# Kernel optimization log

Measured on AMD Instinct MI355X. Metric: run time of the kernel, lower is better.

## Reference

```python
import jax, jax.numpy as jnp
import numpy as np

B, H, W, C, D = 32, 28, 28, 768, 64  # batch, height, width, input_dim, adapter dim
EMB = 64  # meta_net output / layer_embedding size


def qgelu(x):
    return x * jax.nn.sigmoid(1.702 * x)


def setup_inputs() -> dict:
    key = jax.random.key(0)
    ks = jax.random.split(key, 10)
    s = 0.02
    return {
        "x": jax.random.normal(ks[0], (B, H, W, C), jnp.float32),
        "meta_w1": jax.random.normal(ks[1], (EMB, C), jnp.float32) * s,
        "meta_b1": jnp.zeros((EMB,), jnp.float32),
        "meta_w2": jax.random.normal(ks[2], (EMB, EMB), jnp.float32) * s,
        "meta_b2": jnp.zeros((EMB,), jnp.float32),
        "layer_emb": jax.random.normal(ks[3], (EMB,), jnp.float32),
        "hyper_w": jax.random.normal(ks[4], (D * D * 9, EMB), jnp.float32) * s,
        "hyper_b": jnp.zeros((D * D * 9,), jnp.float32),
        "down_w": jax.random.normal(ks[5], (D, C), jnp.float32) * np.sqrt(6.0 / (C + D)),
        "down_b": jnp.zeros((D,), jnp.float32),
        "up_w": jax.random.normal(ks[6], (C, D), jnp.float32) * s,  # torch inits zeros; random for nontrivial test
        "up_b": jnp.zeros((C,), jnp.float32),
    }


def reference(x, meta_w1, meta_b1, meta_w2, meta_b2, layer_emb,
              hyper_w, hyper_b, down_w, down_b, up_w, up_b):
    # meta_net: Linear -> ReLU -> Linear, then mean over (H, W)
    h = jax.nn.relu(jnp.einsum('bhwc,oc->bhwo', x, meta_w1) + meta_b1)
    prompt = (jnp.einsum('bhwo,po->bhwp', h, meta_w2) + meta_b2).mean(axis=(1, 2))  # [B, EMB]
    # fuse_type == 'add'
    fused = layer_emb[None, :] + prompt  # [B, EMB]
    # hypernet -> per-sample conv weights [B, D, D, 3, 3]
    conv_w = (fused @ hyper_w.T + hyper_b).reshape(-1, D, D, 3, 3)
    # adapter_down + QuickGELU
    x_down = jnp.einsum('bhwc,dc->bhwd', x, down_w) + down_b  # [B,H,W,D]
    x_patch = qgelu(x_down).transpose(0, 3, 1, 2)  # [B,D,H,W]
    # per-sample 3x3 conv, stride 1, padding 1 (vmapped over batch)
    def conv1(xi, wi):
        return jax.lax.conv_general_dilated(xi[None], wi, (1, 1), [(1, 1), (1, 1)])[0]
    y = jax.vmap(conv1)(x_patch, conv_w)  # [B,D,H,W]
    y = qgelu(y.transpose(0, 2, 3, 1))  # [B,H,W,D]; dropout is identity in eval
    return jnp.einsum('bhwd,cd->bhwc', y, up_w) + up_b
```

## Files before the change

### kernel.cpp

```cpp
#include <hip/hip_runtime.h>
#include <math.h>

#define B_    32
#define H_    28
#define W_    28
#define C_    768
#define D_    64
#define EMB_  64
#define HW_   (H_ * W_)
#define NPOS  (B_ * HW_)
#define CWROWS (D_ * D_ * 9)

typedef __attribute__((ext_vector_type(8))) short bf16x8;
typedef __attribute__((ext_vector_type(4))) float f32x4;

__device__ __forceinline__ float qgelu(float v) {
    return v / (1.f + __expf(-1.702f * v));
}
__device__ __forceinline__ float relu(float v) { return fmaxf(v, 0.f); }

__device__ __forceinline__ ushort f2bf(float f) {
    union { float f; unsigned u; } v; v.f = f;
    return (ushort)((v.u + 0x7fffu + ((v.u >> 16) & 1u)) >> 16);
}

__device__ __forceinline__ void* swz(void* base, int row, int kbyte) {
    return (void*)((char*)base + row * 128 + (kbyte ^ ((row & 7) << 4)));
}

typedef const __attribute__((address_space(1))) void g_void;
typedef __attribute__((address_space(3))) void l_void;
__device__ __forceinline__ void gload16(const void* g, void* l) {
    __builtin_amdgcn_global_load_lds((g_void*)g, (l_void*)l, 16, 0, 0);
}

__global__ void k_cvt(const float* __restrict__ w1, const float* __restrict__ dw,
                      const float* __restrict__ uw,
                      ushort* __restrict__ wcat2, ushort* __restrict__ wup2)
{
    const int f = (blockIdx.x * 256 + threadIdx.x) * 4;
    float4 v;
    size_t dst;
    ushort* base;
    if (f < 98304) {
        int n, k;
        if (f < 49152) { n = f / 768;            k = f % 768; v = *(const float4*)(w1 + (size_t)n * 768 + k); }
        else           { int g = f - 49152; n = 64 + g / 768; k = g % 768; v = *(const float4*)(dw + (size_t)(n - 64) * 768 + k); }
        const int kb = k >> 6, kk = k & 63;
        dst  = (size_t)kb * 8192 + n * 64 + (kk ^ ((n & 7) << 3));
        base = wcat2;
    } else {
        const int g = f - 98304;
        const int n = g >> 6, kk = g & 63;
        v = *(const float4*)(uw + g);
        dst  = (size_t)n * 64 + (kk ^ ((n & 7) << 3));
        base = wup2;
    }
    union { ushort u[4]; uint2 p; } o;
    o.u[0] = f2bf(v.x); o.u[1] = f2bf(v.y); o.u[2] = f2bf(v.z); o.u[3] = f2bf(v.w);
    *(uint2*)(base + dst) = o.p;
}

__global__ __launch_bounds__(256)
void k_gemm_md(const float* __restrict__ x, const ushort* __restrict__ wcat2,
               const float* __restrict__ b1, const float* __restrict__ db,
               float* __restrict__ hbuf, ushort* __restrict__ xact)
{
    __shared__ ushort As[32 * 64];
    __shared__ ushort Bs[128 * 64];
    const int t = threadIdx.x;
    const int wid = t >> 6, lane = t & 63;
    const int lo = lane & 15, hi = lane >> 4;
    const int bm = blockIdx.x;

    f32x4 acc[2][2] = {};

    const int arow = t >> 3, akq = t & 7;
    const float* asrc = x + (size_t)(bm * 32 + arow) * C_ + akq * 8;

    float4 p0 = *(const float4*)(asrc);
    float4 p1 = *(const float4*)(asrc + 4);

    for (int k0 = 0; k0 < C_; k0 += 64) {
        __syncthreads();
        {
            union { ushort u[8]; float4 v; } tmp;
            tmp.u[0] = f2bf(p0.x); tmp.u[1] = f2bf(p0.y);
            tmp.u[2] = f2bf(p0.z); tmp.u[3] = f2bf(p0.w);
            tmp.u[4] = f2bf(p1.x); tmp.u[5] = f2bf(p1.y);
            tmp.u[6] = f2bf(p1.z); tmp.u[7] = f2bf(p1.w);
            *(float4*)swz(As, arow, akq * 16) = tmp.v;
        }
        {
            const ushort* bsrc = wcat2 + (size_t)(k0 >> 6) * 8192;
            #pragma unroll
            for (int c = 0; c < 4; ++c) {
                const int cbase = (wid * 4 + c) * 512;
                gload16(bsrc + cbase + lane * 8, (ushort*)Bs + cbase);
            }
        }
        if (k0 + 64 < C_) {
            p0 = *(const float4*)(asrc + k0 + 64);
            p1 = *(const float4*)(asrc + k0 + 68);
        }
        __syncthreads();

        #pragma unroll
        for (int ks = 0; ks < 2; ++ks) {
            bf16x8 a[2], b[2];
            #pragma unroll
            for (int i = 0; i < 2; ++i)
                a[i] = *(const bf16x8*)swz(As, i * 16 + lo, ks * 64 + hi * 16);
            #pragma unroll
            for (int j = 0; j < 2; ++j)
                b[j] = *(const bf16x8*)swz(Bs, wid * 32 + j * 16 + lo, ks * 64 + hi * 16);
            #pragma unroll
            for (int i = 0; i < 2; ++i)
                #pragma unroll
                for (int j = 0; j < 2; ++j)
                    acc[i][j] = __builtin_amdgcn_mfma_f32_16x16x32_bf16(a[i], b[j], acc[i][j], 0, 0, 0);
        }
    }

    #pragma unroll
    for (int j = 0; j < 2; ++j) {
        const int n = wid * 32 + j * 16 + lo;
        if (n < 64) {
            const float bias = b1[n];
            #pragma unroll
            for (int i = 0; i < 2; ++i)
                #pragma unroll
                for (int r = 0; r < 4; ++r) {
                    int pos = bm * 32 + i * 16 + hi * 4 + r;
                    hbuf[(size_t)pos * 64 + n] = relu(acc[i][j][r] + bias);
                }
        } else {
            const float bias = db[n - 64];
            #pragma unroll
            for (int i = 0; i < 2; ++i)
                #pragma unroll
                for (int r = 0; r < 4; ++r) {
                    int pos = bm * 32 + i * 16 + hi * 4 + r;
                    xact[(size_t)pos * 64 + (n - 64)] = f2bf(qgelu(acc[i][j][r] + bias));
                }
        }
    }
}

__global__ void k_reduce1(const float* __restrict__ hbuf, float* __restrict__ partial)
{
    __shared__ float part[16][EMB_];
    const int b = blockIdx.x, q = blockIdx.y;
    const int tid = threadIdx.x;
    const int e4 = tid & 15, pc = tid >> 4;

    const float* base = hbuf + ((size_t)b * HW_ + q * 196) * 64 + e4 * 4;
    float4 acc = make_float4(0.f, 0.f, 0.f, 0.f);
    for (int i = pc; i < 196; i += 16) {
        float4 v = *(const float4*)(base + (size_t)i * 64);
        acc.x += v.x; acc.y += v.y; acc.z += v.z; acc.w += v.w;
    }
    part[pc][e4 * 4 + 0] = acc.x;
    part[pc][e4 * 4 + 1] = acc.y;
    part[pc][e4 * 4 + 2] = acc.z;
    part[pc][e4 * 4 + 3] = acc.w;
    __syncthreads();
    if (tid < EMB_) {
        float s = 0.f;
        #pragma unroll
        for (int c = 0; c < 16; ++c) s += part[c][tid];
        partial[(size_t)(b * 4 + q) * EMB_ + tid] = s;
    }
}

__global__ void k_hyper(const float* __restrict__ partial, const float* __restrict__ layer_emb,
                        const float* __restrict__ w2, const float* __restrict__ b2,
                        const float* __restrict__ hyper_w, const float* __restrict__ hyper_b,
                        ushort* __restrict__ cwb)
{
    __shared__ float w2L[64][65];
    __shared__ float hmL[8][EMB_];
    __shared__ float fusedL[8][EMB_];
    const int tid = threadIdx.x;
    const int b0 = blockIdx.y * 8;

    for (int i = tid; i < 1024; i += 256) {
        int r = i >> 4, c = (i & 15) * 4;
        float4 v = *(const float4*)(w2 + (size_t)r * 64 + c);
        w2L[r][c] = v.x; w2L[r][c + 1] = v.y; w2L[r][c + 2] = v.z; w2L[r][c + 3] = v.w;
    }
    for (int i = tid; i < 512; i += 256) {
        int bl = i >> 6, e = i & 63;
        const float* pp = partial + (size_t)((b0 + bl) * 4) * EMB_ + e;
        float s = pp[0] + pp[64] + pp[128] + pp[192];
        hmL[bl][e] = s * (1.f / HW_);
    }
    __syncthreads();
    for (int i = tid; i < 512; i += 256) {
        int bl = i >> 6, e = i & 63;
        float a0 = 0.f, a1 = 0.f, a2 = 0.f, a3 = 0.f;
        #pragma unroll
        for (int k = 0; k < EMB_; k += 4) {
            a0 = fmaf(hmL[bl][k + 0], w2L[e][k + 0], a0);
            a1 = fmaf(hmL[bl][k + 1], w2L[e][k + 1], a1);
            a2 = fmaf(hmL[bl][k + 2], w2L[e][k + 2], a2);
            a3 = fmaf(hmL[bl][k + 3], w2L[e][k + 3], a3);
        }
        fusedL[bl][e] = (a0 + a1) + (a2 + a3) + b2[e] + layer_emb[e];
    }
    __syncthreads();

    const int f    = blockIdx.x * 256 + tid;
    const int din  = f & 63;
    const int dout = (f >> 6) & 63;
    const int tap  = f >> 12;
    const int r    = (dout * 64 + din) * 9 + tap;

    float wrow[EMB_];
    const float4* hw4 = (const float4*)(hyper_w + (size_t)r * EMB_);
    #pragma unroll
    for (int i = 0; i < EMB_ / 4; ++i) {
        float4 v = hw4[i];
        wrow[i*4+0] = v.x; wrow[i*4+1] = v.y; wrow[i*4+2] = v.z; wrow[i*4+3] = v.w;
    }
    const float hb = hyper_b[r];

    for (int bl = 0; bl < 8; ++bl) {
        float a0 = 0.f, a1 = 0.f, a2 = 0.f, a3 = 0.f;
        #pragma unroll
        for (int i = 0; i < EMB_; i += 4) {
            a0 = fmaf(fusedL[bl][i+0], wrow[i+0], a0);
            a1 = fmaf(fusedL[bl][i+1], wrow[i+1], a1);
            a2 = fmaf(fusedL[bl][i+2], wrow[i+2], a2);
            a3 = fmaf(fusedL[bl][i+3], wrow[i+3], a3);
        }
        cwb[(size_t)(b0 + bl) * CWROWS + f] = f2bf((a0 + a1) + (a2 + a3) + hb);
    }
}

__global__ __launch_bounds__(512)
void k_convup(const ushort* __restrict__ xact, const ushort* __restrict__ cwb,
              const ushort* __restrict__ wup2, const float* __restrict__ ub,
              float* __restrict__ out)
{
    __shared__ ushort wsl[192 * 64];
    __shared__ ushort xs[34 * 64];
    const int t = threadIdx.x;
    const int lane = t & 63;
    const int lo = lane & 15, hi = lane >> 4;
    const int b = blockIdx.x / H_;
    const int h = blockIdx.x % H_;
    const int mw = (t >> 6) >> 2;
    const int nw = (t >> 6) & 3;
    const int w0 = mw * 16;

    f32x4 acc = {};

    for (int kh = 0; kh < 3; ++kh) {
        const int hh = h + kh - 1;
        __syncthreads();
        const ushort* wsrc = cwb + (size_t)b * CWROWS + (size_t)kh * 3 * 4096;
        #pragma unroll
        for (int s = 0; s < 3; ++s) {
            int j = s * 512 + t;
            *(float4*)swz(wsl, j >> 3, (j & 7) * 16) = *(const float4*)(wsrc + j * 8);
        }
        if (t < 272) {
            int c = t >> 3, kseg = t & 7;
            int w = c - 1;
            float4 v = make_float4(0.f, 0.f, 0.f, 0.f);
            if (hh >= 0 && hh < H_ && w >= 0 && w < W_)
                v = *(const float4*)(xact + ((size_t)((b * H_ + hh) * W_) + w) * 64 + kseg * 8);
            *(float4*)swz(xs, c, kseg * 16) = v;
        }
        __syncthreads();
        #pragma unroll
        for (int kw = 0; kw < 3; ++kw) {
            #pragma unroll
            for (int ks = 0; ks < 2; ++ks) {
                bf16x8 a  = *(const bf16x8*)swz(xs, w0 + lo + kw, ks * 64 + hi * 16);
                bf16x8 bf = *(const bf16x8*)swz(wsl, kw * 64 + nw * 16 + lo, ks * 64 + hi * 16);
                acc = __builtin_amdgcn_mfma_f32_16x16x32_bf16(a, bf, acc, 0, 0, 0);
            }
        }
    }

    __syncthreads();
    ushort* yt = xs;
    const int dout = nw * 16 + lo;
    #pragma unroll
    for (int r = 0; r < 4; ++r) {
        int w = w0 + hi * 4 + r;
        *(ushort*)swz(yt, w, dout * 2) = f2bf(qgelu(acc[r]));
    }
    __syncthreads();

    bf16x8 af[2];
    #pragma unroll
    for (int ks = 0; ks < 2; ++ks)
        af[ks] = *(const bf16x8*)swz(yt, mw * 16 + lo, ks * 64 + hi * 16);

    ushort* Bs = wsl;
    const size_t pos0 = (size_t)(b * H_ + h) * W_;

    for (int nc = 0; nc < 6; ++nc) {
        {
            const ushort* bsrc = wup2 + (size_t)nc * 8192;
            const int wid = t >> 6;
            #pragma unroll
            for (int c = 0; c < 2; ++c) {
                const int cbase = (wid * 2 + c) * 512;
                gload16(bsrc + cbase + lane * 8, Bs + cbase);
            }
        }
        __syncthreads();

        f32x4 uacc[2] = {};
        #pragma unroll
        for (int ks = 0; ks < 2; ++ks) {
            bf16x8 bb[2];
            #pragma unroll
            for (int j = 0; j < 2; ++j)
                bb[j] = *(const bf16x8*)swz(Bs, nw * 32 + j * 16 + lo, ks * 64 + hi * 16);
            #pragma unroll
            for (int j = 0; j < 2; ++j)
                uacc[j] = __builtin_amdgcn_mfma_f32_16x16x32_bf16(af[ks], bb[j], uacc[j], 0, 0, 0);
        }

        #pragma unroll
        for (int j = 0; j < 2; ++j) {
            const int n = nc * 128 + nw * 32 + j * 16 + lo;
            const float bias = ub[n];
            #pragma unroll
            for (int r = 0; r < 4; ++r) {
                int m = mw * 16 + hi * 4 + r;
                if (m < W_)
                    out[(pos0 + m) * C_ + n] = uacc[j][r] + bias;
            }
        }
        __syncthreads();
    }
}

extern "C" void kernel_launch(void* const* d_in, const int* in_sizes, int n_in,
                              void* d_out, int out_size, void* d_ws, size_t ws_size,
                              hipStream_t stream) {
    const float* x         = (const float*)d_in[0];
    const float* meta_w1   = (const float*)d_in[1];
    const float* meta_b1   = (const float*)d_in[2];
    const float* meta_w2   = (const float*)d_in[3];
    const float* meta_b2   = (const float*)d_in[4];
    const float* layer_emb = (const float*)d_in[5];
    const float* hyper_w   = (const float*)d_in[6];
    const float* hyper_b   = (const float*)d_in[7];
    const float* down_w    = (const float*)d_in[8];
    const float* down_b    = (const float*)d_in[9];
    const float* up_w      = (const float*)d_in[10];
    const float* up_b      = (const float*)d_in[11];
    float* out = (float*)d_out;

    char* p = (char*)d_ws;
    float*  hbuf    = (float*)p;           p += (size_t)NPOS * 64 * 4;
    ushort* xact    = (ushort*)p;          p += (size_t)NPOS * 64 * 2;
    float*  partial = (float*)p;           p += (size_t)B_ * 4 * EMB_ * 4;
    ushort* cwb     = (ushort*)p;          p += (size_t)B_ * CWROWS * 2;
    ushort* wcat2   = (ushort*)p;          p += (size_t)128 * C_ * 2;
    ushort* wup2    = (ushort*)p;

    k_cvt<<<144, 256, 0, stream>>>(meta_w1, down_w, up_w, wcat2, wup2);
    k_gemm_md<<<NPOS / 32, 256, 0, stream>>>(x, wcat2, meta_b1, down_b, hbuf, xact);
    k_reduce1<<<dim3(B_, 4), 256, 0, stream>>>(hbuf, partial);
    dim3 hgrid(CWROWS / 256, B_ / 8);
    k_hyper<<<hgrid, 256, 0, stream>>>(partial, layer_emb, meta_w2, meta_b2,
                                       hyper_w, hyper_b, cwb);
    k_convup<<<B_ * H_, 512, 0, stream>>>(xact, cwb, wup2, up_b, out);
}
```

Before: 70.44 us.

## Double-buffer LDS tiles in down-projection GEMM and up-projection loop

Adds ping-pong shared-memory buffers to the first GEMM kernel and to the up-projection stage of the conv kernel. The next K tile or N chunk is prefetched into the alternate buffer while MFMAs run on the current one, which halves the barriers per iteration and hides global load latency. In exchange it uses more LDS per block, which may lower occupancy, especially in k_convup where an extra 16KB buffer is added.

Measured after the change: 74.93 us. 1.06x slower.

```diff
diff --git a/kernel.cpp b/kernel.cpp
--- a/kernel.cpp
+++ b/kernel.cpp
@@ -61,13 +61,53 @@
     *(uint2*)(base + dst) = o.p;
 }
 
+#define GEMM_STEP(KT, CA, CB, NA, NB)                                              \
+    {                                                                               \
+        __syncthreads();                                                            \
+        const bool more = (KT) < 11;                                                \
+        float4 q0, q1;                                                              \
+        if (more) {                                                                 \
+            q0 = *(const float4*)(asrc + ((KT) + 1) * 64);                          \
+            q1 = *(const float4*)(asrc + ((KT) + 1) * 64 + 4);                      \
+            const ushort* bsrc = wcat2 + (size_t)((KT) + 1) * 8192;                 \
+            _Pragma("unroll")                                                       \
+            for (int c = 0; c < 4; ++c) {                                           \
+                const int cb = (wid * 4 + c) * 512;                                 \
+                gload16(bsrc + cb + lane * 8, (ushort*)(NB) + cb);                  \
+            }                                                                       \
+        }                                                                           \
+        _Pragma("unroll")                                                           \
+        for (int ks = 0; ks < 2; ++ks) {                                            \
+            bf16x8 a[2], b[2];                                                      \
+            _Pragma("unroll")                                                       \
+            for (int i = 0; i < 2; ++i)                                             \
+                a[i] = *(const bf16x8*)swz((CA), i * 16 + lo, ks * 64 + hi * 16);   \
+            _Pragma("unroll")                                                       \
+            for (int j = 0; j < 2; ++j)                                             \
+                b[j] = *(const bf16x8*)swz((CB), wid * 32 + j * 16 + lo, ks * 64 + hi * 16); \
+            _Pragma("unroll")                                                       \
+            for (int i = 0; i < 2; ++i)                                             \
+                _Pragma("unroll")                                                   \
+                for (int j = 0; j < 2; ++j)                                         \
+                    acc[i][j] = __builtin_amdgcn_mfma_f32_16x16x32_bf16(a[i], b[j], acc[i][j], 0, 0, 0); \
+        }                                                                           \
+        if (more) {                                                                 \
+            union { ushort u[8]; float4 v; } tmp;                                   \
+            tmp.u[0] = f2bf(q0.x); tmp.u[1] = f2bf(q0.y);                           \
+            tmp.u[2] = f2bf(q0.z); tmp.u[3] = f2bf(q0.w);                           \
+            tmp.u[4] = f2bf(q1.x); tmp.u[5] = f2bf(q1.y);                           \
+            tmp.u[6] = f2bf(q1.z); tmp.u[7] = f2bf(q1.w);                           \
+            *(float4*)swz((NA), arow, akq * 16) = tmp.v;                            \
+        }                                                                           \
+    }
+
 __global__ __launch_bounds__(256)
 void k_gemm_md(const float* __restrict__ x, const ushort* __restrict__ wcat2,
                const float* __restrict__ b1, const float* __restrict__ db,
                float* __restrict__ hbuf, ushort* __restrict__ xact)
 {
-    __shared__ ushort As[32 * 64];
-    __shared__ ushort Bs[128 * 64];
+    __shared__ ushort As0[32 * 64], As1[32 * 64];
+    __shared__ ushort Bs0[128 * 64], Bs1[128 * 64];
     const int t = threadIdx.x;
     const int wid = t >> 6, lane = t & 63;
     const int lo = lane & 15, hi = lane >> 4;
@@ -78,48 +118,25 @@
     const int arow = t >> 3, akq = t & 7;
     const float* asrc = x + (size_t)(bm * 32 + arow) * C_ + akq * 8;
 
-    float4 p0 = *(const float4*)(asrc);
-    float4 p1 = *(const float4*)(asrc + 4);
-
-    for (int k0 = 0; k0 < C_; k0 += 64) {
-        __syncthreads();
-        {
-            union { ushort u[8]; float4 v; } tmp;
-            tmp.u[0] = f2bf(p0.x); tmp.u[1] = f2bf(p0.y);
-            tmp.u[2] = f2bf(p0.z); tmp.u[3] = f2bf(p0.w);
-            tmp.u[4] = f2bf(p1.x); tmp.u[5] = f2bf(p1.y);
-            tmp.u[6] = f2bf(p1.z); tmp.u[7] = f2bf(p1.w);
-            *(float4*)swz(As, arow, akq * 16) = tmp.v;
-        }
-        {
-            const ushort* bsrc = wcat2 + (size_t)(k0 >> 6) * 8192;
-            #pragma unroll
-            for (int c = 0; c < 4; ++c) {
-                const int cbase = (wid * 4 + c) * 512;
-                gload16(bsrc + cbase + lane * 8, (ushort*)Bs + cbase);
-            }
-        }
-        if (k0 + 64 < C_) {
-            p0 = *(const float4*)(asrc + k0 + 64);
-            p1 = *(const float4*)(asrc + k0 + 68);
-        }
-        __syncthreads();
-
-        #pragma unroll
-        for (int ks = 0; ks < 2; ++ks) {
-            bf16x8 a[2], b[2];
-            #pragma unroll
-            for (int i = 0; i < 2; ++i)
-                a[i] = *(const bf16x8*)swz(As, i * 16 + lo, ks * 64 + hi * 16);
-            #pragma unroll
-            for (int j = 0; j < 2; ++j)
-                b[j] = *(const bf16x8*)swz(Bs, wid * 32 + j * 16 + lo, ks * 64 + hi * 16);
-            #pragma unroll
-            for (int i = 0; i < 2; ++i)
-                #pragma unroll
-                for (int j = 0; j < 2; ++j)
-                    acc[i][j] = __builtin_amdgcn_mfma_f32_16x16x32_bf16(a[i], b[j], acc[i][j], 0, 0, 0);
-        }
+    {
+        float4 p0 = *(const float4*)(asrc);
+        float4 p1 = *(const float4*)(asrc + 4);
+        #pragma unroll
+        for (int c = 0; c < 4; ++c) {
+            const int cb = (wid * 4 + c) * 512;
+            gload16(wcat2 + cb + lane * 8, (ushort*)Bs0 + cb);
+        }
+        union { ushort u[8]; float4 v; } tmp;
+        tmp.u[0] = f2bf(p0.x); tmp.u[1] = f2bf(p0.y);
+        tmp.u[2] = f2bf(p0.z); tmp.u[3] = f2bf(p0.w);
+        tmp.u[4] = f2bf(p1.x); tmp.u[5] = f2bf(p1.y);
+        tmp.u[6] = f2bf(p1.z); tmp.u[7] = f2bf(p1.w);
+        *(float4*)swz(As0, arow, akq * 16) = tmp.v;
+    }
+
+    for (int kt = 0; kt < 12; kt += 2) {
+        GEMM_STEP(kt,     As0, Bs0, As1, Bs1);
+        GEMM_STEP(kt + 1, As1, Bs1, As0, Bs0);
     }
 
     #pragma unroll
@@ -238,12 +255,48 @@
     }
 }
 
+#define UP_STEP(NC, CB, NB)                                                        \
+    {                                                                               \
+        __syncthreads();                                                            \
+        if ((NC) < 5) {                                                             \
+            const ushort* bsrc = wup2 + (size_t)((NC) + 1) * 8192;                  \
+            _Pragma("unroll")                                                       \
+            for (int c = 0; c < 2; ++c) {                                           \
+                const int cb = ((t >> 6) * 2 + c) * 512;                            \
+                gload16(bsrc + cb + lane * 8, (ushort*)(NB) + cb);                  \
+            }                                                                       \
+        }                                                                           \
+        f32x4 uacc[2] = {};                                                         \
+        _Pragma("unroll")                                                           \
+        for (int ks = 0; ks < 2; ++ks) {                                            \
+            bf16x8 bb[2];                                                           \
+            _Pragma("unroll")                                                       \
+            for (int j = 0; j < 2; ++j)                                             \
+                bb[j] = *(const bf16x8*)swz((CB), nw * 32 + j * 16 + lo, ks * 64 + hi * 16); \
+            _Pragma("unroll")                                                       \
+            for (int j = 0; j < 2; ++j)                                             \
+                uacc[j] = __builtin_amdgcn_mfma_f32_16x16x32_bf16(af[ks], bb[j], uacc[j], 0, 0, 0); \
+        }                                                                           \
+        _Pragma("unroll")                                                           \
+        for (int j = 0; j < 2; ++j) {                                               \
+            const int n = (NC) * 128 + nw * 32 + j * 16 + lo;                       \
+            const float bias = ub[n];                                               \
+            _Pragma("unroll")                                                       \
+            for (int r = 0; r < 4; ++r) {                                           \
+                int m = mw * 16 + hi * 4 + r;                                       \
+                if (m < W_)                                                         \
+                    out[(pos0 + m) * C_ + n] = uacc[j][r] + bias;                   \
+            }                                                                       \
+        }                                                                           \
+    }
+
 __global__ __launch_bounds__(512)
 void k_convup(const ushort* __restrict__ xact, const ushort* __restrict__ cwb,
               const ushort* __restrict__ wup2, const float* __restrict__ ub,
               float* __restrict__ out)
 {
     __shared__ ushort wsl[192 * 64];
+    __shared__ ushort bs1[128 * 64];
     __shared__ ushort xs[34 * 64];
     const int t = threadIdx.x;
     const int lane = t & 63;
@@ -295,50 +348,23 @@
     }
     __syncthreads();
 
+    {
+        #pragma unroll
+        for (int c = 0; c < 2; ++c) {
+            const int cb = ((t >> 6) * 2 + c) * 512;
+            gload16(wup2 + cb + lane * 8, (ushort*)wsl + cb);
+        }
+    }
     bf16x8 af[2];
     #pragma unroll
     for (int ks = 0; ks < 2; ++ks)
         af[ks] = *(const bf16x8*)swz(yt, mw * 16 + lo, ks * 64 + hi * 16);
 
-    ushort* Bs = wsl;
     const size_t pos0 = (size_t)(b * H_ + h) * W_;
 
-    for (int nc = 0; nc < 6; ++nc) {
-        {
-            const ushort* bsrc = wup2 + (size_t)nc * 8192;
-            const int wid = t >> 6;
-            #pragma unroll
-            for (int c = 0; c < 2; ++c) {
-                const int cbase = (wid * 2 + c) * 512;
-                gload16(bsrc + cbase + lane * 8, Bs + cbase);
-            }
-        }
-        __syncthreads();
-
-        f32x4 uacc[2] = {};
-        #pragma unroll
-        for (int ks = 0; ks < 2; ++ks) {
-            bf16x8 bb[2];
-            #pragma unroll
-            for (int j = 0; j < 2; ++j)
-                bb[j] = *(const bf16x8*)swz(Bs, nw * 32 + j * 16 + lo, ks * 64 + hi * 16);
-            #pragma unroll
-            for (int j = 0; j < 2; ++j)
-                uacc[j] = __builtin_amdgcn_mfma_f32_16x16x32_bf16(af[ks], bb[j], uacc[j], 0, 0, 0);
-        }
-
-        #pragma unroll
-        for (int j = 0; j < 2; ++j) {
-            const int n = nc * 128 + nw * 32 + j * 16 + lo;
-            const float bias = ub[n];
-            #pragma unroll
-            for (int r = 0; r < 4; ++r) {
-                int m = mw * 16 + hi * 4 + r;
-                if (m < W_)
-                    out[(pos0 + m) * C_ + n] = uacc[j][r] + bias;
-            }
-        }
-        __syncthreads();
+    for (int nc = 0; nc < 6; nc += 2) {
+        UP_STEP(nc,     wsl, bs1);
+        UP_STEP(nc + 1, bs1, wsl);
     }
 }
 
```

## Fuse spatial mean partial sums into GEMM epilogue and drop reduce kernel

Applied to the files above, without the earlier changes.

The relu meta-net outputs are now summed per block inside the GEMM epilogue, split into two partial buffers for blocks that straddle a batch boundary. The k_hyper kernel then gathers these per-block partials. This removes the full-size hbuf write, its read-back, and one kernel launch. In exchange the epilogue gains a shared-memory reduction and a sync, and k_hyper runs a small loop over about 25 partials per sample.

Measured after the change: 79.06 us. 12.2% more time.

```diff
diff --git a/kernel.cpp b/kernel.cpp
--- a/kernel.cpp
+++ b/kernel.cpp
@@ -64,10 +64,13 @@
 __global__ __launch_bounds__(256)
 void k_gemm_md(const float* __restrict__ x, const ushort* __restrict__ wcat2,
                const float* __restrict__ b1, const float* __restrict__ db,
-               float* __restrict__ hbuf, ushort* __restrict__ xact)
+               float* __restrict__ pbufA, float* __restrict__ pbufB,
+               ushort* __restrict__ xact)
 {
     __shared__ ushort As[32 * 64];
     __shared__ ushort Bs[128 * 64];
+    __shared__ float sA[4][64];
+    __shared__ float sB[4][64];
     const int t = threadIdx.x;
     const int wid = t >> 6, lane = t & 63;
     const int lo = lane & 15, hi = lane >> 4;
@@ -122,58 +125,52 @@
         }
     }
 
-    #pragma unroll
-    for (int j = 0; j < 2; ++j) {
-        const int n = wid * 32 + j * 16 + lo;
-        if (n < 64) {
+    if (wid < 2) {
+        const int blo = (bm * 32) / HW_;
+        const int cut = min((blo + 1) * HW_ - bm * 32, 32);
+        #pragma unroll
+        for (int j = 0; j < 2; ++j) {
+            const int n = wid * 32 + j * 16 + lo;
             const float bias = b1[n];
+            float vA = 0.f, vB = 0.f;
+            #pragma unroll
+            for (int i = 0; i < 2; ++i)
+                #pragma unroll
+                for (int r = 0; r < 4; ++r) {
+                    const int p = i * 16 + hi * 4 + r;
+                    float v = relu(acc[i][j][r] + bias);
+                    if (p < cut) vA += v; else vB += v;
+                }
+            sA[hi][n] = vA;
+            sB[hi][n] = vB;
+        }
+    } else {
+        const float bias = db[wid * 32 - 64 + lo];
+        (void)bias;
+        #pragma unroll
+        for (int j = 0; j < 2; ++j) {
+            const int n = wid * 32 + j * 16 + lo;
+            const float bias2 = db[n - 64];
             #pragma unroll
             for (int i = 0; i < 2; ++i)
                 #pragma unroll
                 for (int r = 0; r < 4; ++r) {
                     int pos = bm * 32 + i * 16 + hi * 4 + r;
-                    hbuf[(size_t)pos * 64 + n] = relu(acc[i][j][r] + bias);
+                    xact[(size_t)pos * 64 + (n - 64)] = f2bf(qgelu(acc[i][j][r] + bias2));
                 }
-        } else {
-            const float bias = db[n - 64];
-            #pragma unroll
-            for (int i = 0; i < 2; ++i)
-                #pragma unroll
-                for (int r = 0; r < 4; ++r) {
-                    int pos = bm * 32 + i * 16 + hi * 4 + r;
-                    xact[(size_t)pos * 64 + (n - 64)] = f2bf(qgelu(acc[i][j][r] + bias));
-                }
-        }
-    }
-}
-
-__global__ void k_reduce1(const float* __restrict__ hbuf, float* __restrict__ partial)
-{
-    __shared__ float part[16][EMB_];
-    const int b = blockIdx.x, q = blockIdx.y;
-    const int tid = threadIdx.x;
-    const int e4 = tid & 15, pc = tid >> 4;
-
-    const float* base = hbuf + ((size_t)b * HW_ + q * 196) * 64 + e4 * 4;
-    float4 acc = make_float4(0.f, 0.f, 0.f, 0.f);
-    for (int i = pc; i < 196; i += 16) {
-        float4 v = *(const float4*)(base + (size_t)i * 64);
-        acc.x += v.x; acc.y += v.y; acc.z += v.z; acc.w += v.w;
-    }
-    part[pc][e4 * 4 + 0] = acc.x;
-    part[pc][e4 * 4 + 1] = acc.y;
-    part[pc][e4 * 4 + 2] = acc.z;
-    part[pc][e4 * 4 + 3] = acc.w;
-    __syncthreads();
-    if (tid < EMB_) {
-        float s = 0.f;
-        #pragma unroll
-        for (int c = 0; c < 16; ++c) s += part[c][tid];
-        partial[(size_t)(b * 4 + q) * EMB_ + tid] = s;
-    }
-}
-
-__global__ void k_hyper(const float* __restrict__ partial, const float* __restrict__ layer_emb,
+        }
+    }
+    __syncthreads();
+    if (t < 64)
+        pbufA[(size_t)bm * 64 + t] = sA[0][t] + sA[1][t] + sA[2][t] + sA[3][t];
+    else if (t < 128) {
+        const int e = t - 64;
+        pbufB[(size_t)bm * 64 + e] = sB[0][e] + sB[1][e] + sB[2][e] + sB[3][e];
+    }
+}
+
+__global__ void k_hyper(const float* __restrict__ pbufA, const float* __restrict__ pbufB,
+                        const float* __restrict__ layer_emb,
                         const float* __restrict__ w2, const float* __restrict__ b2,
                         const float* __restrict__ hyper_w, const float* __restrict__ hyper_b,
                         ushort* __restrict__ cwb)
@@ -191,8 +188,15 @@
     }
     for (int i = tid; i < 512; i += 256) {
         int bl = i >> 6, e = i & 63;
-        const float* pp = partial + (size_t)((b0 + bl) * 4) * EMB_ + e;
-        float s = pp[0] + pp[64] + pp[128] + pp[192];
+        const int b = b0 + bl;
+        const int bmS = (b * HW_) >> 5;
+        const int bmE = (b * HW_ + HW_ - 1) >> 5;
+        float s = 0.f;
+        for (int bm = bmS; bm <= bmE; ++bm) {
+            const int blo = (bm * 32) / HW_;
+            s += (blo == b) ? pbufA[(size_t)bm * 64 + e]
+                            : pbufB[(size_t)bm * 64 + e];
+        }
         hmL[bl][e] = s * (1.f / HW_);
     }
     __syncthreads();
@@ -360,18 +364,18 @@
     float* out = (float*)d_out;
 
     char* p = (char*)d_ws;
-    float*  hbuf    = (float*)p;           p += (size_t)NPOS * 64 * 4;
     ushort* xact    = (ushort*)p;          p += (size_t)NPOS * 64 * 2;
-    float*  partial = (float*)p;           p += (size_t)B_ * 4 * EMB_ * 4;
+    float*  pbufA   = (float*)p;           p += (size_t)(NPOS / 32) * 64 * 4;
+    float*  pbufB   = (float*)p;           p += (size_t)(NPOS / 32) * 64 * 4;
     ushort* cwb     = (ushort*)p;          p += (size_t)B_ * CWROWS * 2;
     ushort* wcat2   = (ushort*)p;          p += (size_t)128 * C_ * 2;
     ushort* wup2    = (ushort*)p;
 
     k_cvt<<<144, 256, 0, stream>>>(meta_w1, down_w, up_w, wcat2, wup2);
-    k_gemm_md<<<NPOS / 32, 256, 0, stream>>>(x, wcat2, meta_b1, down_b, hbuf, xact);
-    k_reduce1<<<dim3(B_, 4), 256, 0, stream>>>(hbuf, partial);
+    k_gemm_md<<<NPOS / 32, 256, 0, stream>>>(x, wcat2, meta_b1, down_b,
+                                             pbufA, pbufB, xact);
     dim3 hgrid(CWROWS / 256, B_ / 8);
-    k_hyper<<<hgrid, 256, 0, stream>>>(partial, layer_emb, meta_w2, meta_b2,
+    k_hyper<<<hgrid, 256, 0, stream>>>(pbufA, pbufB, layer_emb, meta_w2, meta_b2,
                                        hyper_w, hyper_b, cwb);
     k_convup<<<B_ * H_, 512, 0, stream>>>(xact, cwb, wup2, up_b, out);
 }
```
